# Performance work log

Hardware: AMD Instinct MI355X
Metric: run time of the kernel (lower is better)

Reference implementation:

```python
import jax, jax.numpy as jnp
from jax import lax
import numpy as np

B, C, H, W = 32, 256, 56, 56
R = max(1, C // 16)  # reduced channels = 16
K = 7                # spatial kernel


def setup_inputs() -> dict:
    key = jax.random.key(0)
    k_x, k1, k2, k3 = jax.random.split(key, 4)
    x = jax.random.normal(k_x, (B, C, H, W), dtype=jnp.float32)
    # shared MLP 1x1 convs (bias=False): stored as 2D matrices
    w1 = jax.random.normal(k1, (R, C), dtype=jnp.float32) * (1.0 / np.sqrt(C))
    w2 = jax.random.normal(k2, (C, R), dtype=jnp.float32) * (1.0 / np.sqrt(R))
    # spatial 7x7 conv: 2 in-channels (avg,max) -> 1 out, OIHW
    w_sp = jax.random.normal(k3, (1, 2, K, K), dtype=jnp.float32) * (1.0 / np.sqrt(2 * K * K))
    return {"x": x, "w1": w1, "w2": w2, "w_sp": w_sp}


def reference(x, w1, w2, w_sp):
    # ---- Channel attention ----
    avg = jnp.mean(x, axis=(2, 3))            # (B, C)
    mx = jnp.max(x, axis=(2, 3))              # (B, C)

    def mlp(v):  # shared 1x1-conv MLP on pooled vectors
        return jnp.einsum('cr,br->bc', w2, jax.nn.relu(jnp.einsum('rc,bc->br', w1, v)))

    ca = jax.nn.sigmoid(mlp(avg) + mlp(mx))[:, :, None, None]  # (B, C, 1, 1)
    xc = x * ca                                # (B, C, H, W)

    # ---- Spatial attention ----
    pooled = jnp.stack([jnp.mean(xc, axis=1), jnp.max(xc, axis=1)], axis=1)  # (B, 2, H, W)
    pad = (K - 1) // 2
    sa = jax.nn.sigmoid(
        lax.conv_general_dilated(pooled, w_sp, window_strides=(1, 1),
                                 padding=[(pad, pad), (pad, pad)],
                                 dimension_numbers=('NCHW', 'OIHW', 'NCHW')))  # (B, 1, H, W)

    # ---- Residual ----
    return x + xc * sa
```

## Files before the change

kernel.cpp:

```cpp
#include <hip/hip_runtime.h>
#include <math.h>

#define B_ 32
#define C_ 256
#define H_ 56
#define W_ 56
#define HW_ (H_*W_)
#define Q_ (HW_/4)
#define R_ 16
#define K_ 7

__device__ __forceinline__ float sigmoidf_(float v) { return 1.0f / (1.0f + expf(-v)); }

__global__ void k_pool_bc(const float* __restrict__ x,
                          float* __restrict__ avg, float* __restrict__ mx) {
    const int bc = blockIdx.x;
    const float4* xp = (const float4*)(x + (size_t)bc * HW_);
    float s = 0.0f, m = -INFINITY;
    for (int i = threadIdx.x; i < Q_; i += blockDim.x) {
        float4 v = xp[i];
        s += v.x + v.y + v.z + v.w;
        m = fmaxf(m, fmaxf(fmaxf(v.x, v.y), fmaxf(v.z, v.w)));
    }
    #pragma unroll
    for (int off = 32; off > 0; off >>= 1) {
        s += __shfl_down(s, off, 64);
        m  = fmaxf(m, __shfl_down(m, off, 64));
    }
    __shared__ float ss[4], sm[4];
    const int wave = threadIdx.x >> 6;
    if ((threadIdx.x & 63) == 0) { ss[wave] = s; sm[wave] = m; }
    __syncthreads();
    if (threadIdx.x == 0) {
        float S = ss[0] + ss[1] + ss[2] + ss[3];
        float M = fmaxf(fmaxf(sm[0], sm[1]), fmaxf(sm[2], sm[3]));
        avg[bc] = S * (1.0f / HW_);
        mx[bc]  = M;
    }
}

__global__ void k_mlp_ca(const float* __restrict__ avg, const float* __restrict__ mx,
                         const float* __restrict__ w1, const float* __restrict__ w2,
                         float* __restrict__ ca) {
    const int b = blockIdx.x;
    __shared__ float sa_[C_], sm_[C_], h_[R_];
    const int t = threadIdx.x;
    sa_[t] = avg[b * C_ + t];
    sm_[t] = mx[b * C_ + t];
    __syncthreads();
    if (t < R_) {
        float ha = 0.0f, hm = 0.0f;
        for (int c = 0; c < C_; ++c) {
            const float wv = w1[t * C_ + c];
            ha += wv * sa_[c];
            hm += wv * sm_[c];
        }
        h_[t] = fmaxf(ha, 0.0f) + fmaxf(hm, 0.0f);
    }
    __syncthreads();
    float acc = 0.0f;
    #pragma unroll
    for (int r = 0; r < R_; ++r) acc += w2[t * R_ + r] * h_[r];
    ca[b * C_ + t] = sigmoidf_(acc);
}

__global__ void __launch_bounds__(256)
k_spatial_pool(const float* __restrict__ x, const float* __restrict__ ca,
               float* __restrict__ pooled) {
    const int b  = blockIdx.y;
    const int q0 = blockIdx.x * 16;
    const int t  = threadIdx.x;
    const int tq = t & 15;
    const int tc = t >> 4;
    const int q  = q0 + tq;

    const float4* xp = (const float4*)(x + (size_t)b * C_ * HW_);
    const float* cab = ca + b * C_;

    float4 s = {0.f, 0.f, 0.f, 0.f};
    float4 m = {-INFINITY, -INFINITY, -INFINITY, -INFINITY};
    #pragma unroll 4
    for (int i = 0; i < 16; ++i) {
        const int c = tc * 16 + i;
        const float a = cab[c];
        float4 v = xp[(size_t)c * Q_ + q];
        v.x *= a; v.y *= a; v.z *= a; v.w *= a;
        s.x += v.x; s.y += v.y; s.z += v.z; s.w += v.w;
        m.x = fmaxf(m.x, v.x); m.y = fmaxf(m.y, v.y);
        m.z = fmaxf(m.z, v.z); m.w = fmaxf(m.w, v.w);
    }

    __shared__ float4 ls[256];
    __shared__ float4 lm[256];
    ls[t] = s; lm[t] = m;
    __syncthreads();
    #pragma unroll
    for (int st = 8; st >= 1; st >>= 1) {
        if (tc < st) {
            const int o = t + st * 16;
            float4 os = ls[o], om = lm[o];
            s.x += os.x; s.y += os.y; s.z += os.z; s.w += os.w;
            m.x = fmaxf(m.x, om.x); m.y = fmaxf(m.y, om.y);
            m.z = fmaxf(m.z, om.z); m.w = fmaxf(m.w, om.w);
            ls[t] = s; lm[t] = m;
        }
        __syncthreads();
    }
    if (tc == 0) {
        const float inv = 1.0f / C_;
        float4 sm4 = {s.x * inv, s.y * inv, s.z * inv, s.w * inv};
        ((float4*)(pooled + (size_t)b * 2 * HW_))[q]       = sm4;
        ((float4*)(pooled + (size_t)b * 2 * HW_ + HW_))[q] = m;
    }
}

__global__ void k_conv_sa(const float* __restrict__ pooled, const float* __restrict__ wsp,
                          float* __restrict__ sa) {
    __shared__ float wv[2 * K_ * K_];
    if (threadIdx.x < 2 * K_ * K_) wv[threadIdx.x] = wsp[threadIdx.x];
    __syncthreads();
    const int idx = blockIdx.x * blockDim.x + threadIdx.x;
    if (idx >= B_ * HW_) return;
    const int b = idx / HW_;
    const int hw = idx % HW_;
    const int h = hw / W_, w = hw % W_;
    const float* pa = pooled + (size_t)b * 2 * HW_;
    const float* pm = pa + HW_;
    float acc = 0.0f;
    #pragma unroll
    for (int ky = 0; ky < K_; ++ky) {
        const int y = h + ky - 3;
        if (y < 0 || y >= H_) continue;
        #pragma unroll
        for (int kx = 0; kx < K_; ++kx) {
            const int xx = w + kx - 3;
            if (xx < 0 || xx >= W_) continue;
            const int o = y * W_ + xx;
            acc += wv[ky * K_ + kx] * pa[o] + wv[K_ * K_ + ky * K_ + kx] * pm[o];
        }
    }
    sa[idx] = sigmoidf_(acc);
}

__global__ void k_finalize(const float* __restrict__ x, const float* __restrict__ ca,
                           const float* __restrict__ sa, float* __restrict__ out) {
    const size_t idx = (size_t)blockIdx.x * blockDim.x + threadIdx.x;
    if (idx >= (size_t)B_ * C_ * Q_) return;
    const size_t e = idx * 4;
    const int b  = (int)(e / ((size_t)C_ * HW_));
    const int c  = (int)((e / HW_) % C_);
    const int hw = (int)(e % HW_);
    const float a = ca[b * C_ + c];
    const float4 s4 = *(const float4*)(sa + (size_t)b * HW_ + hw);
    const float4 v  = *(const float4*)(x + e);
    float4 o;
    o.x = v.x * (1.0f + a * s4.x);
    o.y = v.y * (1.0f + a * s4.y);
    o.z = v.z * (1.0f + a * s4.z);
    o.w = v.w * (1.0f + a * s4.w);
    *(float4*)((float*)out + e) = o;
}

extern "C" void kernel_launch(void* const* d_in, const int* in_sizes, int n_in,
                              void* d_out, int out_size, void* d_ws, size_t ws_size,
                              hipStream_t stream) {
    const float* x   = (const float*)d_in[0];
    const float* w1  = (const float*)d_in[1];
    const float* w2  = (const float*)d_in[2];
    const float* wsp = (const float*)d_in[3];
    float* out = (float*)d_out;

    float* ws     = (float*)d_ws;
    float* avg    = ws;
    float* mx     = avg + B_ * C_;
    float* ca     = mx + B_ * C_;
    float* pooled = ca + B_ * C_;
    float* sa     = pooled + (size_t)B_ * 2 * HW_;

    k_pool_bc<<<B_ * C_, 256, 0, stream>>>(x, avg, mx);
    k_mlp_ca<<<B_, C_, 0, stream>>>(avg, mx, w1, w2, ca);
    {
        dim3 g(Q_ / 16, B_);
        k_spatial_pool<<<g, 256, 0, stream>>>(x, ca, pooled);
    }
    {
        const int n = B_ * HW_;
        k_conv_sa<<<(n + 255) / 256, 256, 0, stream>>>(pooled, wsp, sa);
    }
    {
        const size_t n = (size_t)B_ * C_ * Q_;
        k_finalize<<<(int)((n + 255) / 256), 256, 0, stream>>>(x, ca, sa, out);
    }
}
```

Measured before the change: 233.3 us.

## Fuse channel MLP into pooling via last-block atomic and fuse conv into finalize

Channel pooling and the shared MLP become one kernel. Each block bumps an atomic counter, and the last block to finish computes the channel attention for all batches. The spatial 7x7 conv is merged into the final elementwise pass, with each block computing sigmoid attention for two rows in shared memory before scaling x, so the intermediate sa buffer and two launches go away. The cost is that the MLP now runs serially in a single block, plus an extra memset launch for the counter.

```diff
diff --git a/kernel.cpp b/kernel.cpp
--- a/kernel.cpp
+++ b/kernel.cpp
@@ -7,17 +7,22 @@
 #define W_ 56
 #define HW_ (H_*W_)
 #define Q_ (HW_/4)
+#define W4_ (W_/4)
 #define R_ 16
 #define K_ 7
+#define KK_ (K_*K_)
 
 __device__ __forceinline__ float sigmoidf_(float v) { return 1.0f / (1.0f + expf(-v)); }
 
-__global__ void k_pool_bc(const float* __restrict__ x,
-                          float* __restrict__ avg, float* __restrict__ mx) {
+__global__ void __launch_bounds__(256)
+k_pool_mlp(const float* __restrict__ x, const float* __restrict__ w1,
+           const float* __restrict__ w2, float* __restrict__ avg,
+           float* __restrict__ mx, float* __restrict__ ca,
+           unsigned* __restrict__ cnt) {
     const int bc = blockIdx.x;
     const float4* xp = (const float4*)(x + (size_t)bc * HW_);
     float s = 0.0f, m = -INFINITY;
-    for (int i = threadIdx.x; i < Q_; i += blockDim.x) {
+    for (int i = threadIdx.x; i < Q_; i += 256) {
         float4 v = xp[i];
         s += v.x + v.y + v.z + v.w;
         m = fmaxf(m, fmaxf(fmaxf(v.x, v.y), fmaxf(v.z, v.w)));
@@ -28,40 +33,51 @@
         m  = fmaxf(m, __shfl_down(m, off, 64));
     }
     __shared__ float ss[4], sm[4];
+    __shared__ int lastFlag;
     const int wave = threadIdx.x >> 6;
     if ((threadIdx.x & 63) == 0) { ss[wave] = s; sm[wave] = m; }
     __syncthreads();
     if (threadIdx.x == 0) {
         float S = ss[0] + ss[1] + ss[2] + ss[3];
         float M = fmaxf(fmaxf(sm[0], sm[1]), fmaxf(sm[2], sm[3]));
-        avg[bc] = S * (1.0f / HW_);
-        mx[bc]  = M;
-    }
-}
-
-__global__ void k_mlp_ca(const float* __restrict__ avg, const float* __restrict__ mx,
-                         const float* __restrict__ w1, const float* __restrict__ w2,
-                         float* __restrict__ ca) {
-    const int b = blockIdx.x;
-    __shared__ float sa_[C_], sm_[C_], h_[R_];
+        __hip_atomic_store(&avg[bc], S * (1.0f / HW_), __ATOMIC_RELAXED, __HIP_MEMORY_SCOPE_AGENT);
+        __hip_atomic_store(&mx[bc],  M,                __ATOMIC_RELAXED, __HIP_MEMORY_SCOPE_AGENT);
+        unsigned old = __hip_atomic_fetch_add(cnt, 1u, __ATOMIC_ACQ_REL, __HIP_MEMORY_SCOPE_AGENT);
+        lastFlag = (old == (unsigned)(gridDim.x - 1)) ? 1 : 0;
+    }
+    __syncthreads();
+    if (!lastFlag) return;
+
+    __shared__ float sv[8][2 * C_];
+    __shared__ float sh[B_][R_];
     const int t = threadIdx.x;
-    sa_[t] = avg[b * C_ + t];
-    sm_[t] = mx[b * C_ + t];
-    __syncthreads();
-    if (t < R_) {
-        float ha = 0.0f, hm = 0.0f;
-        for (int c = 0; c < C_; ++c) {
-            const float wv = w1[t * C_ + c];
-            ha += wv * sa_[c];
-            hm += wv * sm_[c];
-        }
-        h_[t] = fmaxf(ha, 0.0f) + fmaxf(hm, 0.0f);
-    }
-    __syncthreads();
-    float acc = 0.0f;
-    #pragma unroll
-    for (int r = 0; r < R_; ++r) acc += w2[t * R_ + r] * h_[r];
-    ca[b * C_ + t] = sigmoidf_(acc);
+    for (int g = 0; g < 4; ++g) {
+        for (int i = t; i < 8 * C_; i += 256) {
+            const int bb = i / C_, c = i % C_;
+            const int b = g * 8 + bb;
+            sv[bb][c]      = __hip_atomic_load(&avg[b * C_ + c], __ATOMIC_RELAXED, __HIP_MEMORY_SCOPE_AGENT);
+            sv[bb][C_ + c] = __hip_atomic_load(&mx[b * C_ + c],  __ATOMIC_RELAXED, __HIP_MEMORY_SCOPE_AGENT);
+        }
+        __syncthreads();
+        if (t < 8 * R_) {
+            const int bb = t / R_, r = t % R_;
+            float ha = 0.0f, hm = 0.0f;
+            for (int c = 0; c < C_; ++c) {
+                const float wv = w1[r * C_ + c];
+                ha += wv * sv[bb][c];
+                hm += wv * sv[bb][C_ + c];
+            }
+            sh[g * 8 + bb][r] = fmaxf(ha, 0.0f) + fmaxf(hm, 0.0f);
+        }
+        __syncthreads();
+    }
+    for (int k = t; k < B_ * C_; k += 256) {
+        const int b = k / C_, c = k % C_;
+        float acc = 0.0f;
+        #pragma unroll
+        for (int r = 0; r < R_; ++r) acc += w2[c * R_ + r] * sh[b][r];
+        ca[k] = sigmoidf_(acc);
+    }
 }
 
 __global__ void __launch_bounds__(256)
@@ -114,51 +130,61 @@
     }
 }
 
-__global__ void k_conv_sa(const float* __restrict__ pooled, const float* __restrict__ wsp,
-                          float* __restrict__ sa) {
-    __shared__ float wv[2 * K_ * K_];
-    if (threadIdx.x < 2 * K_ * K_) wv[threadIdx.x] = wsp[threadIdx.x];
-    __syncthreads();
-    const int idx = blockIdx.x * blockDim.x + threadIdx.x;
-    if (idx >= B_ * HW_) return;
-    const int b = idx / HW_;
-    const int hw = idx % HW_;
-    const int h = hw / W_, w = hw % W_;
-    const float* pa = pooled + (size_t)b * 2 * HW_;
-    const float* pm = pa + HW_;
-    float acc = 0.0f;
-    #pragma unroll
-    for (int ky = 0; ky < K_; ++ky) {
-        const int y = h + ky - 3;
-        if (y < 0 || y >= H_) continue;
+__global__ void __launch_bounds__(256)
+k_conv_final(const float* __restrict__ x, const float* __restrict__ pooled,
+             const float* __restrict__ wsp, const float* __restrict__ ca,
+             float* __restrict__ out) {
+    const int b  = blockIdx.y;
+    const int h0 = blockIdx.x * 2;
+    const int t  = threadIdx.x;
+    __shared__ float wv[2 * KK_];
+    __shared__ float s_sa[2 * W_];
+    __shared__ float s_ca[C_];
+    if (t < 2 * KK_) wv[t] = wsp[t];
+    if (t < C_) s_ca[t] = ca[b * C_ + t];
+    __syncthreads();
+    if (t < 2 * W_) {
+        const int row = t / W_;
+        const int w   = t % W_;
+        const int h   = h0 + row;
+        const float* pa = pooled + (size_t)b * 2 * HW_;
+        const float* pm = pa + HW_;
+        float acc = 0.0f;
         #pragma unroll
-        for (int kx = 0; kx < K_; ++kx) {
-            const int xx = w + kx - 3;
-            if (xx < 0 || xx >= W_) continue;
-            const int o = y * W_ + xx;
-            acc += wv[ky * K_ + kx] * pa[o] + wv[K_ * K_ + ky * K_ + kx] * pm[o];
-        }
-    }
-    sa[idx] = sigmoidf_(acc);
-}
-
-__global__ void k_finalize(const float* __restrict__ x, const float* __restrict__ ca,
-                           const float* __restrict__ sa, float* __restrict__ out) {
-    const size_t idx = (size_t)blockIdx.x * blockDim.x + threadIdx.x;
-    if (idx >= (size_t)B_ * C_ * Q_) return;
-    const size_t e = idx * 4;
-    const int b  = (int)(e / ((size_t)C_ * HW_));
-    const int c  = (int)((e / HW_) % C_);
-    const int hw = (int)(e % HW_);
-    const float a = ca[b * C_ + c];
-    const float4 s4 = *(const float4*)(sa + (size_t)b * HW_ + hw);
-    const float4 v  = *(const float4*)(x + e);
-    float4 o;
-    o.x = v.x * (1.0f + a * s4.x);
-    o.y = v.y * (1.0f + a * s4.y);
-    o.z = v.z * (1.0f + a * s4.z);
-    o.w = v.w * (1.0f + a * s4.w);
-    *(float4*)((float*)out + e) = o;
+        for (int ky = 0; ky < K_; ++ky) {
+            const int y = h + ky - 3;
+            if (y < 0 || y >= H_) continue;
+            #pragma unroll
+            for (int kx = 0; kx < K_; ++kx) {
+                const int xx = w + kx - 3;
+                if (xx < 0 || xx >= W_) continue;
+                const int o = y * W_ + xx;
+                acc += wv[ky * K_ + kx] * pa[o] + wv[KK_ + ky * K_ + kx] * pm[o];
+            }
+        }
+        s_sa[t] = sigmoidf_(acc);
+    }
+    __syncthreads();
+    const float4* xr   = (const float4*)(x + (size_t)b * C_ * HW_ + h0 * W_);
+    float4*       outr = (float4*)((float*)out + (size_t)b * C_ * HW_ + h0 * W_);
+    #pragma unroll 4
+    for (int i = 0; i < 28; ++i) {
+        const int j   = i * 256 + t;
+        const int c   = j / 28;
+        const int rem = j % 28;
+        const int row = rem / W4_;
+        const int w4  = rem % W4_;
+        const size_t off4 = (size_t)c * (HW_ / 4) + row * W4_ + w4;
+        const float4 v  = xr[off4];
+        const float  a  = s_ca[c];
+        const float4 sa4 = *(const float4*)&s_sa[row * W_ + w4 * 4];
+        float4 o;
+        o.x = v.x * (1.0f + a * sa4.x);
+        o.y = v.y * (1.0f + a * sa4.y);
+        o.z = v.z * (1.0f + a * sa4.z);
+        o.w = v.w * (1.0f + a * sa4.w);
+        outr[off4] = o;
+    }
 }
 
 extern "C" void kernel_launch(void* const* d_in, const int* in_sizes, int n_in,
@@ -175,20 +201,17 @@
     float* mx     = avg + B_ * C_;
     float* ca     = mx + B_ * C_;
     float* pooled = ca + B_ * C_;
-    float* sa     = pooled + (size_t)B_ * 2 * HW_;
-
-    k_pool_bc<<<B_ * C_, 256, 0, stream>>>(x, avg, mx);
-    k_mlp_ca<<<B_, C_, 0, stream>>>(avg, mx, w1, w2, ca);
+    unsigned* cnt = (unsigned*)(pooled + (size_t)B_ * 2 * HW_);
+
+    hipMemsetAsync(cnt, 0, sizeof(unsigned), stream);
+
+    k_pool_mlp<<<B_ * C_, 256, 0, stream>>>(x, w1, w2, avg, mx, ca, cnt);
     {
         dim3 g(Q_ / 16, B_);
         k_spatial_pool<<<g, 256, 0, stream>>>(x, ca, pooled);
     }
     {
-        const int n = B_ * HW_;
-        k_conv_sa<<<(n + 255) / 256, 256, 0, stream>>>(pooled, wsp, sa);
-    }
-    {
-        const size_t n = (size_t)B_ * C_ * Q_;
-        k_finalize<<<(int)((n + 255) / 256), 256, 0, stream>>>(x, ca, sa, out);
-    }
-}
+        dim3 g(H_ / 2, B_);
+        k_conv_final<<<g, 256, 0, stream>>>(x, pooled, wsp, ca, out);
+    }
+}
```

Measured after the change: 521.4 us. 124% more time.
